# Performance work log

Measured on AMD Instinct MI355X. Metric: run time of the kernel, lower is better.

## Reference

```python
import jax, jax.numpy as jnp
import numpy as np

B, I, R, L, U = 256, 512, 1024, 2, 11  # batch, input_size, rnn_size, num_layers, num_unroll


def setup_inputs() -> dict:
    key = jax.random.key(0)
    ks = jax.random.split(key, 10)
    s = 0.02
    return {
        "x": jax.random.normal(ks[0], (B, I), jnp.float32),
        "init_states_input": jax.random.normal(ks[1], (B, 2 * L * R), jnp.float32),
        # per-unroll (NOT shared) weights, stacked along unroll dim U
        "Wi0": jax.random.normal(ks[2], (U, 4 * R, I), jnp.float32) * s,
        "bi0": jax.random.normal(ks[3], (U, 4 * R), jnp.float32) * s,
        "Wh0": jax.random.normal(ks[4], (U, 4 * R, R), jnp.float32) * s,
        "bh0": jax.random.normal(ks[5], (U, 4 * R), jnp.float32) * s,
        "Wi1": jax.random.normal(ks[6], (U, 4 * R, R), jnp.float32) * s,
        "bi1": jax.random.normal(ks[7], (U, 4 * R), jnp.float32) * s,
        "Wh1": jax.random.normal(ks[8], (U, 4 * R, R), jnp.float32) * s,
        "bh1": jax.random.normal(ks[9], (U, 4 * R), jnp.float32) * s,
    }


def _cell(pre, c_prev):
    # torch chunk(4, dim=1) order: in_gate, forget_gate, out_gate, in_transform
    i, f, o, g = jnp.split(pre, 4, axis=1)
    c = jax.nn.sigmoid(f) * c_prev + jax.nn.sigmoid(i) * jnp.tanh(g)
    h = jax.nn.sigmoid(o) * jnp.tanh(c)
    return h, c


def reference(x, init_states_input, Wi0, bi0, Wh0, bh0, Wi1, bi1, Wh1, bh1):
    st = init_states_input.reshape(B, 2 * L, R)
    # chunk order: [h0, c0, h1, c1]
    h0, c0, h1, c1 = st[:, 0], st[:, 1], st[:, 2], st[:, 3]

    def step(carry, p):
        h0, c0, h1, c1 = carry
        wi0, vbi0, wh0, vbh0, wi1, vbi1, wh1, vbh1 = p
        out_prev = h1  # original appends now_hs[i][-1]: top-layer h BEFORE this step
        pre0 = x @ wi0.T + vbi0 + h0 @ wh0.T + vbh0  # [B, 4R]
        h0n, c0n = _cell(pre0, c0)
        pre1 = h0n @ wi1.T + vbi1 + h1 @ wh1.T + vbh1
        h1n, c1n = _cell(pre1, c1)
        return (h0n, c0n, h1n, c1n), out_prev

    _, ys = jax.lax.scan(step, (h0, c0, h1, c1),
                         (Wi0, bi0, Wh0, bh0, Wi1, bi1, Wh1, bh1))
    # ys: [U, B, R]; torch.cat along dim 1 in unroll order -> [B, U*R]
    return jnp.transpose(ys, (1, 0, 2)).reshape(B, U * R)
```

## Files before the change

### kernel.cpp

```cpp
#include <hip/hip_runtime.h>
#include <hip/hip_bf16.h>

#define B_N 256
#define R_N 1024
#define U_N 11
#define BK 32
#define SP 40

typedef __attribute__((ext_vector_type(8))) short bf16x8;
typedef __attribute__((ext_vector_type(4))) float f32x4;

__device__ __forceinline__ float sigmoid_f(float x) {
    return 1.0f / (1.0f + __expf(-x));
}

__device__ __forceinline__ float tanh_f(float x) {
    x = fminf(15.0f, fmaxf(-15.0f, x));
    const float e = __expf(2.0f * x);
    return (e - 1.0f) / (e + 1.0f);
}

__device__ __forceinline__ short bf16_of(float x) {
    union { __hip_bfloat16 h; short s; } u;
    u.h = __float2bfloat16(x);
    return u.s;
}

__device__ __forceinline__ short4 pack4(float4 v) {
    short4 r;
    r.x = bf16_of(v.x); r.y = bf16_of(v.y);
    r.z = bf16_of(v.z); r.w = bf16_of(v.w);
    return r;
}

__global__ __launch_bounds__(512) void lstm_layer(
    const float* __restrict__ A1, int lda1, int K1, const float* __restrict__ W1,
    const float* __restrict__ A2, int lda2, int K2, const float* __restrict__ W2,
    const float* __restrict__ bi, const float* __restrict__ bh,
    float* __restrict__ c_state,
    float* __restrict__ h_out, int ldh)
{
    __shared__ __align__(16) short sA[2][32 * SP];
    __shared__ __align__(16) short sW[2][128 * SP];
    __shared__ float sPre[2][4 * 32 * 32];

    const int tid  = threadIdx.x;
    const int lane = tid & 63;
    const int wave = tid >> 6;
    const int group = wave >> 2;
    const int gate  = wave & 3;
    const int ln   = lane & 15;
    const int quad = lane >> 4;
    const int lk   = quad * 8;
    const int tg   = tid & 255;

    const int m_base = blockIdx.y * 32;
    const int rb     = blockIdx.x * 32;

    const int Ktot  = K1 + K2;
    const int Khalf = Ktot >> 1;
    const int NC    = Khalf / BK;

    const int arow = tg >> 3;
    const int acol = (tg & 7) * 4;

    f32x4 acc[2][2];
#pragma unroll
    for (int mf = 0; mf < 2; ++mf)
#pragma unroll
        for (int rf = 0; rf < 2; ++rf) {
            f32x4 z = {0.0f, 0.0f, 0.0f, 0.0f};
            acc[mf][rf] = z;
        }

    float4 pA;
    float4 pW[4];

    auto load_chunk = [&](int c) {
        const int kv = group * Khalf + c * BK;
        const float* Ap; int lda; const float* Wp; int ldw; int kc;
        if (kv < K1) { Ap = A1; lda = lda1; Wp = W1; ldw = K1; kc = kv; }
        else         { Ap = A2; lda = lda2; Wp = W2; ldw = K2; kc = kv - K1; }
        pA = *reinterpret_cast<const float4*>(
            Ap + (size_t)(m_base + arow) * lda + kc + acol);
#pragma unroll
        for (int l = 0; l < 4; ++l) {
            const int wrow = l * 32 + (tg >> 3);
            const int g = wrow >> 5, rr = wrow & 31;
            pW[l] = *reinterpret_cast<const float4*>(
                Wp + (size_t)(g * R_N + rb + rr) * ldw + kc + acol);
        }
    };

    auto store_chunk = [&]() {
        *reinterpret_cast<short4*>(&sA[group][arow * SP + acol]) = pack4(pA);
#pragma unroll
        for (int l = 0; l < 4; ++l) {
            const int wrow = l * 32 + (tg >> 3);
            *reinterpret_cast<short4*>(&sW[group][wrow * SP + acol]) = pack4(pW[l]);
        }
    };

    load_chunk(0);
#pragma unroll 1
    for (int c = 0; c < NC; ++c) {
        __syncthreads();
        store_chunk();
        if (c + 1 < NC) load_chunk(c + 1);
        __syncthreads();

        bf16x8 af[2], wf[2];
#pragma unroll
        for (int mf = 0; mf < 2; ++mf)
            af[mf] = *reinterpret_cast<const bf16x8*>(
                &sA[group][(mf * 16 + ln) * SP + lk]);
#pragma unroll
        for (int rf = 0; rf < 2; ++rf)
            wf[rf] = *reinterpret_cast<const bf16x8*>(
                &sW[group][(gate * 32 + rf * 16 + ln) * SP + lk]);

        acc[0][0] = __builtin_amdgcn_mfma_f32_16x16x32_bf16(af[0], wf[0], acc[0][0], 0, 0, 0);
        acc[1][0] = __builtin_amdgcn_mfma_f32_16x16x32_bf16(af[1], wf[0], acc[1][0], 0, 0, 0);
        acc[0][1] = __builtin_amdgcn_mfma_f32_16x16x32_bf16(af[0], wf[1], acc[0][1], 0, 0, 0);
        acc[1][1] = __builtin_amdgcn_mfma_f32_16x16x32_bf16(af[1], wf[1], acc[1][1], 0, 0, 0);
    }

#pragma unroll
    for (int mf = 0; mf < 2; ++mf)
#pragma unroll
        for (int rf = 0; rf < 2; ++rf)
#pragma unroll
            for (int t = 0; t < 4; ++t) {
                const int m = mf * 16 + quad * 4 + t;
                const int r = rf * 16 + ln;
                sPre[group][(gate * 32 + m) * 32 + r] = acc[mf][rf][t];
            }
    __syncthreads();

#pragma unroll
    for (int i = 0; i < 2; ++i) {
        const int ci = tid + i * 512;
        const int m = ci >> 5;
        const int r = ci & 31;
        const int gm = m_base + m;
        const int gr = rb + r;
        const float pI = sPre[0][(0 * 32 + m) * 32 + r] + sPre[1][(0 * 32 + m) * 32 + r]
                       + bi[0 * R_N + gr] + bh[0 * R_N + gr];
        const float pF = sPre[0][(1 * 32 + m) * 32 + r] + sPre[1][(1 * 32 + m) * 32 + r]
                       + bi[1 * R_N + gr] + bh[1 * R_N + gr];
        const float pO = sPre[0][(2 * 32 + m) * 32 + r] + sPre[1][(2 * 32 + m) * 32 + r]
                       + bi[2 * R_N + gr] + bh[2 * R_N + gr];
        const float pG = sPre[0][(3 * 32 + m) * 32 + r] + sPre[1][(3 * 32 + m) * 32 + r]
                       + bi[3 * R_N + gr] + bh[3 * R_N + gr];
        const size_t cidx = (size_t)gm * R_N + gr;
        const float cv = sigmoid_f(pF) * c_state[cidx] + sigmoid_f(pI) * tanh_f(pG);
        c_state[cidx] = cv;
        h_out[(size_t)gm * ldh + gr] = sigmoid_f(pO) * tanh_f(cv);
    }
}

__global__ __launch_bounds__(256) void init_states(
    const float* __restrict__ st, float* __restrict__ h0,
    float* __restrict__ c0, float* __restrict__ c1, float* __restrict__ out)
{
    const int idx = blockIdx.x * 256 + threadIdx.x;
    const int b = idx >> 10;
    const int r = idx & 1023;
    const float* s = st + (size_t)b * 4096;
    h0[idx] = s[r];
    c0[idx] = s[1024 + r];
    out[(size_t)b * (U_N * R_N) + r] = s[2048 + r];
    c1[idx] = s[3072 + r];
}

extern "C" void kernel_launch(void* const* d_in, const int* in_sizes, int n_in,
                              void* d_out, int out_size, void* d_ws, size_t ws_size,
                              hipStream_t stream)
{
    const float* x   = (const float*)d_in[0];
    const float* st  = (const float*)d_in[1];
    const float* Wi0 = (const float*)d_in[2];
    const float* bi0 = (const float*)d_in[3];
    const float* Wh0 = (const float*)d_in[4];
    const float* bh0 = (const float*)d_in[5];
    const float* Wi1 = (const float*)d_in[6];
    const float* bi1 = (const float*)d_in[7];
    const float* Wh1 = (const float*)d_in[8];
    const float* bh1 = (const float*)d_in[9];
    float* out = (float*)d_out;

    float* h0a = (float*)d_ws;
    float* h0b = h0a + B_N * R_N;
    float* c0  = h0b + B_N * R_N;
    float* c1  = c0 + B_N * R_N;

    init_states<<<dim3((B_N * R_N) / 256), 256, 0, stream>>>(st, h0a, c0, c1, out);

    const dim3 grid(R_N / 32, B_N / 32);
    for (int u = 0; u < 10; ++u) {
        const float* h0_in = (u & 1) ? h0b : h0a;
        float* h0_out      = (u & 1) ? h0a : h0b;
        lstm_layer<<<grid, 512, 0, stream>>>(
            x, 512, 512, Wi0 + (size_t)u * 4096 * 512,
            h0_in, R_N, R_N, Wh0 + (size_t)u * 4096 * 1024,
            bi0 + (size_t)u * 4096, bh0 + (size_t)u * 4096,
            c0, h0_out, R_N);
        lstm_layer<<<grid, 512, 0, stream>>>(
            h0_out, R_N, R_N, Wi1 + (size_t)u * 4096 * 1024,
            out + (size_t)u * R_N, U_N * R_N, R_N, Wh1 + (size_t)u * 4096 * 1024,
            bi1 + (size_t)u * 4096, bh1 + (size_t)u * 4096,
            c1, out + (size_t)(u + 1) * R_N, U_N * R_N);
    }
}
```

Before: 1.235 ms.

## Halve hidden-column tile per block and double-buffer LDS with one barrier per chunk

Each block now covers 16 hidden units instead of 32, which doubles the grid so more blocks run on the GPU, and launch bounds request 4 blocks per CU. The K loop ping-pongs two LDS buffers and drops to a single __syncthreads per chunk, and base pointers are precomputed. The per-gate sPre reduction area reuses the staging memory. Each block still loads its own copy of the A tile, so activation traffic doubles, and each wave issues fewer MFMAs per sync.

```diff
diff --git a/kernel.cpp b/kernel.cpp
--- a/kernel.cpp
+++ b/kernel.cpp
@@ -33,16 +33,14 @@
     return r;
 }
 
-__global__ __launch_bounds__(512) void lstm_layer(
+__global__ __launch_bounds__(512, 4) void lstm_layer(
     const float* __restrict__ A1, int lda1, int K1, const float* __restrict__ W1,
     const float* __restrict__ A2, int lda2, int K2, const float* __restrict__ W2,
     const float* __restrict__ bi, const float* __restrict__ bh,
     float* __restrict__ c_state,
     float* __restrict__ h_out, int ldh)
 {
-    __shared__ __align__(16) short sA[2][32 * SP];
-    __shared__ __align__(16) short sW[2][128 * SP];
-    __shared__ float sPre[2][4 * 32 * 32];
+    __shared__ __align__(16) char smem_raw[30720];
 
     const int tid  = threadIdx.x;
     const int lane = tid & 63;
@@ -55,7 +53,7 @@
     const int tg   = tid & 255;
 
     const int m_base = blockIdx.y * 32;
-    const int rb     = blockIdx.x * 32;
+    const int rb     = blockIdx.x * 16;
 
     const int Ktot  = K1 + K2;
     const int Khalf = Ktot >> 1;
@@ -64,93 +62,99 @@
     const int arow = tg >> 3;
     const int acol = (tg & 7) * 4;
 
-    f32x4 acc[2][2];
-#pragma unroll
-    for (int mf = 0; mf < 2; ++mf)
-#pragma unroll
-        for (int rf = 0; rf < 2; ++rf) {
-            f32x4 z = {0.0f, 0.0f, 0.0f, 0.0f};
-            acc[mf][rf] = z;
-        }
+    const float* baseA1 = A1 + (size_t)(m_base + arow) * lda1 + acol;
+    const float* baseA2 = A2 + (size_t)(m_base + arow) * lda2 + acol;
+    const float* baseW1[2];
+    const float* baseW2[2];
+#pragma unroll
+    for (int l = 0; l < 2; ++l) {
+        const int wrow = l * 32 + (tg >> 3);
+        const int g = wrow >> 4, rr = wrow & 15;
+        baseW1[l] = W1 + (size_t)(g * R_N + rb + rr) * K1 + acol;
+        baseW2[l] = W2 + (size_t)(g * R_N + rb + rr) * K2 + acol;
+    }
+
+    f32x4 acc[2];
+#pragma unroll
+    for (int mf = 0; mf < 2; ++mf) {
+        f32x4 z = {0.0f, 0.0f, 0.0f, 0.0f};
+        acc[mf] = z;
+    }
 
     float4 pA;
-    float4 pW[4];
-
+    float4 pW[2];
     auto load_chunk = [&](int c) {
         const int kv = group * Khalf + c * BK;
-        const float* Ap; int lda; const float* Wp; int ldw; int kc;
-        if (kv < K1) { Ap = A1; lda = lda1; Wp = W1; ldw = K1; kc = kv; }
-        else         { Ap = A2; lda = lda2; Wp = W2; ldw = K2; kc = kv - K1; }
-        pA = *reinterpret_cast<const float4*>(
-            Ap + (size_t)(m_base + arow) * lda + kc + acol);
-#pragma unroll
-        for (int l = 0; l < 4; ++l) {
-            const int wrow = l * 32 + (tg >> 3);
-            const int g = wrow >> 5, rr = wrow & 31;
-            pW[l] = *reinterpret_cast<const float4*>(
-                Wp + (size_t)(g * R_N + rb + rr) * ldw + kc + acol);
+        if (kv < K1) {
+            pA = *reinterpret_cast<const float4*>(baseA1 + kv);
+#pragma unroll
+            for (int l = 0; l < 2; ++l)
+                pW[l] = *reinterpret_cast<const float4*>(baseW1[l] + kv);
+        } else {
+            const int kc = kv - K1;
+            pA = *reinterpret_cast<const float4*>(baseA2 + kc);
+#pragma unroll
+            for (int l = 0; l < 2; ++l)
+                pW[l] = *reinterpret_cast<const float4*>(baseW2[l] + kc);
         }
     };
 
-    auto store_chunk = [&]() {
-        *reinterpret_cast<short4*>(&sA[group][arow * SP + acol]) = pack4(pA);
-#pragma unroll
-        for (int l = 0; l < 4; ++l) {
+    auto body = [&](int c, int buf) {
+        short* sAb = reinterpret_cast<short*>(&smem_raw[(size_t)(buf * 2 + group) * 2560]);
+        short* sWb = reinterpret_cast<short*>(&smem_raw[10240 + (size_t)(buf * 2 + group) * 5120]);
+
+        *reinterpret_cast<short4*>(&sAb[arow * SP + acol]) = pack4(pA);
+#pragma unroll
+        for (int l = 0; l < 2; ++l) {
             const int wrow = l * 32 + (tg >> 3);
-            *reinterpret_cast<short4*>(&sW[group][wrow * SP + acol]) = pack4(pW[l]);
+            *reinterpret_cast<short4*>(&sWb[wrow * SP + acol]) = pack4(pW[l]);
         }
+
+        __syncthreads();
+
+        if (c + 1 < NC) load_chunk(c + 1);
+
+        bf16x8 af[2], wf;
+#pragma unroll
+        for (int mf = 0; mf < 2; ++mf)
+            af[mf] = *reinterpret_cast<const bf16x8*>(&sAb[(mf * 16 + ln) * SP + lk]);
+        wf = *reinterpret_cast<const bf16x8*>(&sWb[(gate * 16 + ln) * SP + lk]);
+
+        acc[0] = __builtin_amdgcn_mfma_f32_16x16x32_bf16(af[0], wf, acc[0], 0, 0, 0);
+        acc[1] = __builtin_amdgcn_mfma_f32_16x16x32_bf16(af[1], wf, acc[1], 0, 0, 0);
     };
 
     load_chunk(0);
 #pragma unroll 1
-    for (int c = 0; c < NC; ++c) {
-        __syncthreads();
-        store_chunk();
-        if (c + 1 < NC) load_chunk(c + 1);
-        __syncthreads();
-
-        bf16x8 af[2], wf[2];
-#pragma unroll
-        for (int mf = 0; mf < 2; ++mf)
-            af[mf] = *reinterpret_cast<const bf16x8*>(
-                &sA[group][(mf * 16 + ln) * SP + lk]);
-#pragma unroll
-        for (int rf = 0; rf < 2; ++rf)
-            wf[rf] = *reinterpret_cast<const bf16x8*>(
-                &sW[group][(gate * 32 + rf * 16 + ln) * SP + lk]);
-
-        acc[0][0] = __builtin_amdgcn_mfma_f32_16x16x32_bf16(af[0], wf[0], acc[0][0], 0, 0, 0);
-        acc[1][0] = __builtin_amdgcn_mfma_f32_16x16x32_bf16(af[1], wf[0], acc[1][0], 0, 0, 0);
-        acc[0][1] = __builtin_amdgcn_mfma_f32_16x16x32_bf16(af[0], wf[1], acc[0][1], 0, 0, 0);
-        acc[1][1] = __builtin_amdgcn_mfma_f32_16x16x32_bf16(af[1], wf[1], acc[1][1], 0, 0, 0);
-    }
+    for (int c = 0; c < NC; c += 2) {
+        body(c, 0);
+        body(c + 1, 1);
+    }
+
+    __syncthreads();
+    float* sPre = reinterpret_cast<float*>(smem_raw);
 
 #pragma unroll
     for (int mf = 0; mf < 2; ++mf)
 #pragma unroll
-        for (int rf = 0; rf < 2; ++rf)
-#pragma unroll
-            for (int t = 0; t < 4; ++t) {
-                const int m = mf * 16 + quad * 4 + t;
-                const int r = rf * 16 + ln;
-                sPre[group][(gate * 32 + m) * 32 + r] = acc[mf][rf][t];
-            }
+        for (int t = 0; t < 4; ++t) {
+            const int m = mf * 16 + quad * 4 + t;
+            sPre[group * 2048 + (gate * 32 + m) * 16 + ln] = acc[mf][t];
+        }
     __syncthreads();
 
-#pragma unroll
-    for (int i = 0; i < 2; ++i) {
-        const int ci = tid + i * 512;
-        const int m = ci >> 5;
-        const int r = ci & 31;
+    {
+        const int m = tid >> 4;
+        const int r = tid & 15;
         const int gm = m_base + m;
         const int gr = rb + r;
-        const float pI = sPre[0][(0 * 32 + m) * 32 + r] + sPre[1][(0 * 32 + m) * 32 + r]
+        const float pI = sPre[(0 * 32 + m) * 16 + r] + sPre[2048 + (0 * 32 + m) * 16 + r]
                        + bi[0 * R_N + gr] + bh[0 * R_N + gr];
-        const float pF = sPre[0][(1 * 32 + m) * 32 + r] + sPre[1][(1 * 32 + m) * 32 + r]
+        const float pF = sPre[(1 * 32 + m) * 16 + r] + sPre[2048 + (1 * 32 + m) * 16 + r]
                        + bi[1 * R_N + gr] + bh[1 * R_N + gr];
-        const float pO = sPre[0][(2 * 32 + m) * 32 + r] + sPre[1][(2 * 32 + m) * 32 + r]
+        const float pO = sPre[(2 * 32 + m) * 16 + r] + sPre[2048 + (2 * 32 + m) * 16 + r]
                        + bi[2 * R_N + gr] + bh[2 * R_N + gr];
-        const float pG = sPre[0][(3 * 32 + m) * 32 + r] + sPre[1][(3 * 32 + m) * 32 + r]
+        const float pG = sPre[(3 * 32 + m) * 16 + r] + sPre[2048 + (3 * 32 + m) * 16 + r]
                        + bi[3 * R_N + gr] + bh[3 * R_N + gr];
         const size_t cidx = (size_t)gm * R_N + gr;
         const float cv = sigmoid_f(pF) * c_state[cidx] + sigmoid_f(pI) * tanh_f(pG);
@@ -196,7 +200,7 @@
 
     init_states<<<dim3((B_N * R_N) / 256), 256, 0, stream>>>(st, h0a, c0, c1, out);
 
-    const dim3 grid(R_N / 32, B_N / 32);
+    const dim3 grid(R_N / 16, B_N / 32);
     for (int u = 0; u < 10; ++u) {
         const float* h0_in = (u & 1) ? h0b : h0a;
         float* h0_out      = (u & 1) ? h0a : h0b;
```

Measured after the change: 1.450 ms. 17.4% more time.
